# Kernel optimization log

Measured on AMD Instinct MI355X. Metric: run time of the kernel, lower is better.

## Reference

```python
import jax, jax.numpy as jnp
import numpy as np

MATRIC_TYPE = 0   # 0: corr, 1: cov
WEIGHT_IN = 1.0
WEIGHT_BET = 1.0


def setup_inputs() -> dict:
    key = jax.random.key(0)
    k1, k2, k3 = jax.random.split(key, 3)
    x = jax.random.normal(k1, (256, 128, 768), dtype=jnp.float32)
    label = jax.random.randint(k2, (256,), 0, 1000, dtype=jnp.int64 if jax.config.read('jax_enable_x64') else jnp.int32)
    genre_label = jax.random.randint(k3, (256,), 0, 8, dtype=jnp.int64 if jax.config.read('jax_enable_x64') else jnp.int32)
    return {"x": x, "label": label, "genre_label": genre_label}


def _compute_various(x):
    # x: [B, N, D] -> within (D,D), between (D,D)
    B, N, D = x.shape
    tol_num = B * N
    x_mean = jnp.mean(x, axis=1)                       # (B, D)
    mean = jnp.mean(x.reshape(-1, D), axis=0)          # (D,)
    res_x = x - x_mean[:, None, :]                     # (B, N, D)
    # fused batched scatter accumulation (replaces python loop of small mms)
    within = jnp.einsum('bnd,bne->de', res_x, res_x) / tol_num
    res_mean = x_mean - mean                           # (B, D)
    between = (N * (res_mean.T @ res_mean)) / tol_num
    return within, between


def _corr_normalize(m):
    # torch code: Diag=(d,1); mm(Diag.T, Diag)=(1,1) scalar = sum(diag^2)
    d = jnp.diagonal(m)
    s = jnp.sqrt(jnp.sum(d * d))
    return m / s


def reference(x, label, genre_label):
    input_x = x[::2]
    input_u = x[1::2]
    x1_within, x1_between = _compute_various(input_x)
    x2_within, x2_between = _compute_various(input_u)
    if MATRIC_TYPE == 0:
        x1_within = _corr_normalize(x1_within)
        x2_within = _corr_normalize(x2_within)
        x1_between = _corr_normalize(x1_between)
        x2_between = _corr_normalize(x2_between)
    within = jnp.sum((x1_within - x2_within) ** 2)
    between = jnp.sum((x1_between - x2_between) ** 2)
    return WEIGHT_IN * within + WEIGHT_BET * between
```

## Files before the change

### kernel.cpp

```cpp
#include <hip/hip_runtime.h>


typedef float f32x2 __attribute__((ext_vector_type(2)));
typedef float f32x4 __attribute__((ext_vector_type(4)));
typedef short bf16x8 __attribute__((ext_vector_type(8)));
typedef unsigned short u16x4 __attribute__((ext_vector_type(4)));

static constexpr size_t OFF_RT    = 0;
static constexpr size_t OFF_XM    = 50331648;
static constexpr size_t OFF_M     = 51118080;
static constexpr size_t OFF_RM    = 51124224;
static constexpr size_t OFF_P2    = 51517440;
static constexpr size_t OFF_BPART = 54269952;
static constexpr size_t OFF_P1    = 54355968;

__device__ __forceinline__ unsigned int f2bf_u32(float f) {
  union { float f; unsigned int u; } v; v.f = f;
  unsigned int u = v.u;
  unsigned int lsb = (u >> 16) & 1u;
  u += 0x7fffu + lsb;
  return u >> 16;
}

__device__ __forceinline__ void gload_lds16(const void* g, void* l) {
  __builtin_amdgcn_global_load_lds(
      (const __attribute__((address_space(1))) unsigned int*)g,
      (__attribute__((address_space(3))) unsigned int*)l, 16, 0, 0);
}

__global__ void __launch_bounds__(256) k1_means_convert(const float* __restrict__ x,
                                                        float* __restrict__ xm,
                                                        unsigned short* __restrict__ RT) {
  __shared__ unsigned short T[128][130];
  __shared__ float pm[4][128];
  int bid = blockIdx.x;
  int dt = bid % 6, borig = bid / 6;
  int s = borig & 1, b = borig >> 1;
  int tid = threadIdx.x, w = tid >> 6, lane = tid & 63;

  const float* xb = x + (size_t)borig * (128 * 768) + dt * 128 + 2 * lane;
  float cs0 = 0.f, cs1 = 0.f;
#pragma unroll
  for (int g = 0; g < 8; ++g) {
    int n0 = w * 32 + g * 4;
    f32x2 a0 = *reinterpret_cast<const f32x2*>(xb + (size_t)(n0 + 0) * 768);
    f32x2 a1 = *reinterpret_cast<const f32x2*>(xb + (size_t)(n0 + 1) * 768);
    f32x2 a2 = *reinterpret_cast<const f32x2*>(xb + (size_t)(n0 + 2) * 768);
    f32x2 a3 = *reinterpret_cast<const f32x2*>(xb + (size_t)(n0 + 3) * 768);
    cs0 += a0[0] + a1[0] + a2[0] + a3[0];
    cs1 += a0[1] + a1[1] + a2[1] + a3[1];
    u16x4 p0, p1;
    p0[0] = (unsigned short)f2bf_u32(a0[0]); p0[1] = (unsigned short)f2bf_u32(a1[0]);
    p0[2] = (unsigned short)f2bf_u32(a2[0]); p0[3] = (unsigned short)f2bf_u32(a3[0]);
    p1[0] = (unsigned short)f2bf_u32(a0[1]); p1[1] = (unsigned short)f2bf_u32(a1[1]);
    p1[2] = (unsigned short)f2bf_u32(a2[1]); p1[3] = (unsigned short)f2bf_u32(a3[1]);
    *reinterpret_cast<u16x4*>(&T[2 * lane + 0][n0]) = p0;
    *reinterpret_cast<u16x4*>(&T[2 * lane + 1][n0]) = p1;
  }
  *reinterpret_cast<f32x2*>(&pm[w][2 * lane]) = f32x2{cs0, cs1};
  __syncthreads();

  if (tid < 128) {
    float mv = (pm[0][tid] + pm[1][tid] + pm[2][tid] + pm[3][tid]) * (1.f / 128.f);
    xm[((size_t)(s * 128 + b)) * 768ull + dt * 128 + tid] = mv;
  }

  int half = lane >> 5;
  int nb = (lane & 31) * 4;
  unsigned short* rtbase = RT + (size_t)s * (768ull * 16384ull) + (size_t)(b * 128 + nb);
#pragma unroll
  for (int i = 0; i < 16; ++i) {
    int d_loc = w * 32 + 2 * i + half;
    uint2 v = *reinterpret_cast<const uint2*>(&T[d_loc][nb]);
    *reinterpret_cast<uint2*>(rtbase + (size_t)(dt * 128 + d_loc) * 16384ull) = v;
  }
}

__global__ void __launch_bounds__(256) k2_slice_mean(const float* __restrict__ xm,
                                                     float* __restrict__ m,
                                                     unsigned short* __restrict__ rmT) {
  __shared__ float pm[4][64];
  __shared__ float ml[64];
  int s = blockIdx.x / 12, dg = blockIdx.x % 12;
  int t = threadIdx.x;
  int d_loc = t & 63, part = t >> 6;
  int d = dg * 64 + d_loc;
  const float* base = xm + (size_t)s * 128ull * 768ull + d;
  float acc = 0.f;
#pragma unroll 4
  for (int i = 0; i < 32; ++i) acc += base[(size_t)(part * 32 + i) * 768ull];
  pm[part][d_loc] = acc;
  __syncthreads();
  if (t < 64) {
    float mv = (pm[0][t] + pm[1][t] + pm[2][t] + pm[3][t]) * (1.f / 128.f);
    m[s * 768 + dg * 64 + t] = mv;
    ml[t] = mv;
  }
  __syncthreads();
  float mv = ml[d_loc];
  unsigned short* rt = rmT + ((size_t)s * 768ull + d) * 128ull + part * 32;
#pragma unroll 4
  for (int i = 0; i < 32; ++i)
    rt[i] = (unsigned short)f2bf_u32(base[(size_t)(part * 32 + i) * 768ull] - mv);
}

__device__ __forceinline__ void stage_tile(const unsigned short* __restrict__ g, int KP, int k0,
                                           unsigned short* lds, int wave, int lane) {
#pragma unroll
  for (int i = 0; i < 4; ++i) {
    int cb = (i * 4 + wave) * 64;
    int chunk = cb + lane;
    int r = chunk >> 3, sl = chunk & 7;
    int ss = sl ^ (r & 7);
    const unsigned short* src = g + (size_t)r * KP + (k0 + ss * 8);
    gload_lds16(src, lds + (size_t)cb * 8);
  }
}

__device__ __forceinline__ bf16x8 read_frag(const unsigned short* lds, int row, int slot) {
  int chunk = row * 8 + (slot ^ (row & 7));
  return *reinterpret_cast<const bf16x8*>(lds + chunk * 8);
}

__device__ __forceinline__ void tp2tile(int tp, int& td, int& te) {
  td = 0; int t2 = tp;
  while (t2 >= 6 - td) { t2 -= 6 - td; ++td; }
  te = td + t2;
}

__global__ void __launch_bounds__(256) gemm_ata(const unsigned short* __restrict__ Rbig,
                                                const unsigned short* __restrict__ rmT,
                                                float* __restrict__ P1, float* __restrict__ P2,
                                                int ksplit) {
  __shared__ unsigned short Ta[2][128 * 64];
  __shared__ unsigned short Tb[2][128 * 64];
  int bid = blockIdx.x;
  const unsigned short* R; size_t slice_stride; int KP;
  int rest, step0, step1; float* pout;
  if (bid < 42 * ksplit) {
    R = Rbig; slice_stride = 768ull * 16384ull; KP = 16384;
    int c = bid % ksplit; rest = bid / ksplit;
    step0 = (256 * c) / ksplit; step1 = (256 * (c + 1)) / ksplit;
    pout = P1 + (size_t)bid * (128 * 128);
  } else {
    int b2 = bid - 42 * ksplit;
    R = rmT; slice_stride = 768ull * 128ull; KP = 128;
    rest = b2; step0 = 0; step1 = 2;
    pout = P2 + (size_t)b2 * (128 * 128);
  }
  int s = rest & 1; int tp = rest >> 1;
  int td, te; tp2tile(tp, td, te);
  bool diag = (td == te);
  const unsigned short* Ra = R + (size_t)s * slice_stride + (size_t)(td * 128) * KP;
  const unsigned short* Rb = R + (size_t)s * slice_stride + (size_t)(te * 128) * KP;
  int tid = threadIdx.x, wave = tid >> 6, lane = tid & 63;
  int m_off = (wave >> 1) * 64, n_off = (wave & 1) * 64;
  int row_a = m_off + (lane & 15), row_b = n_off + (lane & 15);
  f32x4 acc[4][4];
#pragma unroll
  for (int i = 0; i < 4; ++i)
#pragma unroll
    for (int j = 0; j < 4; ++j) { acc[i][j][0]=0.f; acc[i][j][1]=0.f; acc[i][j][2]=0.f; acc[i][j][3]=0.f; }

  stage_tile(Ra, KP, step0 * 64, Ta[0], wave, lane);
  if (!diag) stage_tile(Rb, KP, step0 * 64, Tb[0], wave, lane);
  __syncthreads();

  int cur = 0;
  for (int kt = step0; kt < step1; ++kt) {
    if (kt + 1 < step1) {
      stage_tile(Ra, KP, (kt + 1) * 64, Ta[cur ^ 1], wave, lane);
      if (!diag) stage_tile(Rb, KP, (kt + 1) * 64, Tb[cur ^ 1], wave, lane);
    }
    const unsigned short* Bsrc = diag ? Ta[cur] : Tb[cur];
#pragma unroll
    for (int ks = 0; ks < 2; ++ks) {
      bf16x8 a[4], b[4];
      int slot = ks * 4 + (lane >> 4);
#pragma unroll
      for (int mi = 0; mi < 4; ++mi) a[mi] = read_frag(Ta[cur], row_a + mi * 16, slot);
#pragma unroll
      for (int ni = 0; ni < 4; ++ni) b[ni] = read_frag(Bsrc, row_b + ni * 16, slot);
#pragma unroll
      for (int mi = 0; mi < 4; ++mi)
#pragma unroll
        for (int ni = 0; ni < 4; ++ni)
          acc[mi][ni] = __builtin_amdgcn_mfma_f32_16x16x32_bf16(a[mi], b[ni], acc[mi][ni], 0, 0, 0);
    }
    __syncthreads();
    cur ^= 1;
  }
  int hi = lane >> 4, lo = lane & 15;
#pragma unroll
  for (int mi = 0; mi < 4; ++mi)
#pragma unroll
    for (int ni = 0; ni < 4; ++ni)
#pragma unroll
      for (int r = 0; r < 4; ++r) {
        int rr = m_off + mi * 16 + hi * 4 + r;
        int cc = n_off + ni * 16 + lo;
        pout[rr * 128 + cc] = acc[mi][ni][r];
      }
}

template <int KS>
__global__ void __launch_bounds__(256) k5_elem(const float* __restrict__ P1,
                                               const float* __restrict__ P2,
                                               const float* __restrict__ m,
                                               float* __restrict__ bpart, int ksplit_rt) {
  __shared__ float red[4][10];
  int bid = blockIdx.x;
  int tp = bid >> 5, sub = bid & 31;
  int td, te; tp2tile(tp, td, te);
  bool diagTile = (td == te);
  float mult = diagTile ? 1.0f : 2.0f;
  int t = threadIdx.x;
  int lane = t & 63, w = t >> 6;
  int ksplit = (KS > 0) ? KS : ksplit_rt;
  float v[10];
#pragma unroll
  for (int j = 0; j < 10; ++j) v[j] = 0.f;

#pragma unroll
  for (int k = 0; k < 2; ++k) {
    int idx = sub * 512 + k * 256 + t;
    int r = idx >> 7, cc = idx & 127;
    int d = td * 128 + r, e = te * 128 + cc;
    float W[2], B[2];
#pragma unroll
    for (int s = 0; s < 2; ++s) {
      const float* base1 = P1 + (size_t)((tp * 2 + s) * ksplit) * 16384ull + idx;
      float g1 = 0.f;
#pragma unroll
      for (int c6 = 0; c6 < ((KS > 0) ? KS : 16); ++c6) {
        if (KS > 0 || c6 < ksplit) g1 += base1[(size_t)c6 * 16384ull];
      }
      float p2v = P2[(size_t)(tp * 2 + s) * 16384ull + idx];
      W[s] = g1 - 128.0f * p2v - 16384.0f * m[s * 768 + d] * m[s * 768 + e];
      B[s] = p2v;
    }
    v[0] += W[0] * W[0] * mult;  v[1] += W[1] * W[1] * mult;  v[2] += W[0] * W[1] * mult;
    v[3] += B[0] * B[0] * mult;  v[4] += B[1] * B[1] * mult;  v[5] += B[0] * B[1] * mult;
    if (diagTile && r == cc) {
      v[6] += W[0] * W[0];  v[7] += W[1] * W[1];
      v[8] += B[0] * B[0];  v[9] += B[1] * B[1];
    }
  }
#pragma unroll
  for (int off = 32; off; off >>= 1)
#pragma unroll
    for (int j = 0; j < 10; ++j) v[j] += __shfl_down(v[j], off, 64);
  if (lane == 0)
#pragma unroll
    for (int j = 0; j < 10; ++j) red[w][j] = v[j];
  __syncthreads();
  if (t < 10) bpart[bid * 16 + t] = red[0][t] + red[1][t] + red[2][t] + red[3][t];
}

__global__ void __launch_bounds__(256) k6_final(const float* __restrict__ bpart,
                                                float* __restrict__ out) {
  __shared__ float red[4][10];
  float acc[10];
#pragma unroll
  for (int j = 0; j < 10; ++j) acc[j] = 0.f;
  for (int i = threadIdx.x; i < 672; i += 256)
#pragma unroll
    for (int j = 0; j < 10; ++j) acc[j] += bpart[i * 16 + j];
  int lane = threadIdx.x & 63, w = threadIdx.x >> 6;
#pragma unroll
  for (int off = 32; off; off >>= 1)
#pragma unroll
    for (int j = 0; j < 10; ++j) acc[j] += __shfl_down(acc[j], off, 64);
  if (lane == 0)
#pragma unroll
    for (int j = 0; j < 10; ++j) red[w][j] = acc[j];
  __syncthreads();
  if (threadIdx.x == 0) {
    float S[10];
#pragma unroll
    for (int j = 0; j < 10; ++j) S[j] = red[0][j] + red[1][j] + red[2][j] + red[3][j];
    float lw = S[0] / S[6] + S[1] / S[7] - 2.0f * S[2] / sqrtf(S[6] * S[7]);
    float lb = S[3] / S[8] + S[4] / S[9] - 2.0f * S[5] / sqrtf(S[8] * S[9]);
    out[0] = lw + lb;
  }
}

extern "C" void kernel_launch(void* const* d_in, const int* in_sizes, int n_in,
                              void* d_out, int out_size, void* d_ws, size_t ws_size,
                              hipStream_t stream) {
  const float* x = (const float*)d_in[0];
  char* ws = (char*)d_ws;
  unsigned short* RT  = (unsigned short*)(ws + OFF_RT);
  float* xm           = (float*)(ws + OFF_XM);
  float* m            = (float*)(ws + OFF_M);
  unsigned short* rmT = (unsigned short*)(ws + OFF_RM);
  float* P2           = (float*)(ws + OFF_P2);
  float* bpart        = (float*)(ws + OFF_BPART);
  float* P1           = (float*)(ws + OFF_P1);
  float* out          = (float*)d_out;

  size_t availP1 = (ws_size > OFF_P1) ? (ws_size - OFF_P1) : 0;
  int ksplit = (int)(availP1 / (42ull * 128 * 128 * 4));
  if (ksplit > 11) ksplit = 11;
  if (ksplit < 1) ksplit = 1;

  hipLaunchKernelGGL(k1_means_convert, dim3(1536), dim3(256), 0, stream, x, xm, RT);
  hipLaunchKernelGGL(k2_slice_mean, dim3(24), dim3(256), 0, stream, xm, m, rmT);
  hipLaunchKernelGGL(gemm_ata, dim3(42 * ksplit + 42), dim3(256), 0, stream,
                     RT, rmT, P1, P2, ksplit);
  if (ksplit == 11) {
    hipLaunchKernelGGL((k5_elem<11>), dim3(672), dim3(256), 0, stream,
                       P1, P2, m, bpart, ksplit);
  } else {
    hipLaunchKernelGGL((k5_elem<0>), dim3(672), dim3(256), 0, stream,
                       P1, P2, m, bpart, ksplit);
  }
  hipLaunchKernelGGL(k6_final, dim3(1), dim3(256), 0, stream, bpart, out);
}
```

Measured before the change: 77.48 us.

## Retile mean/convert kernel so each block writes wider contiguous transposed rows

Each block of the first kernel now covers 32 feature columns across 4 batches (same slice parity) instead of 128 columns of one batch. The transposed bf16 tile is therefore 32 rows by 512 tokens, so the global stores become 16-byte contiguous runs of 1 KB per row rather than 8-byte writes of 256 bytes. The per-column means are reduced with wavefront shuffles instead of a shared-memory partial sum. The cost is narrower 8-byte global reads per lane (16 lanes per row) and a different LDS padding whose bank conflicts may change.

```diff
diff --git a/kernel.cpp b/kernel.cpp
--- a/kernel.cpp
+++ b/kernel.cpp
@@ -31,18 +31,20 @@
 __global__ void __launch_bounds__(256) k1_means_convert(const float* __restrict__ x,
                                                         float* __restrict__ xm,
                                                         unsigned short* __restrict__ RT) {
-  __shared__ unsigned short T[128][130];
-  __shared__ float pm[4][128];
+  __shared__ unsigned short T[32][536];
   int bid = blockIdx.x;
-  int dt = bid % 6, borig = bid / 6;
-  int s = borig & 1, b = borig >> 1;
-  int tid = threadIdx.x, w = tid >> 6, lane = tid & 63;
-
-  const float* xb = x + (size_t)borig * (128 * 768) + dt * 128 + 2 * lane;
+  int dt = bid % 24, rest = bid / 24;
+  int s = rest & 1, bg = rest >> 1;
+  int tid = threadIdx.x, j = tid >> 6, lane = tid & 63;
+  int p = lane & 15, q = lane >> 4;
+  int d0 = dt * 32;
+  int borig = 8 * bg + 2 * j + s;
+
+  const float* xb = x + (size_t)borig * (128 * 768) + d0 + 2 * p;
   float cs0 = 0.f, cs1 = 0.f;
 #pragma unroll
-  for (int g = 0; g < 8; ++g) {
-    int n0 = w * 32 + g * 4;
+  for (int i = 0; i < 8; ++i) {
+    int n0 = i * 16 + q * 4;
     f32x2 a0 = *reinterpret_cast<const f32x2*>(xb + (size_t)(n0 + 0) * 768);
     f32x2 a1 = *reinterpret_cast<const f32x2*>(xb + (size_t)(n0 + 1) * 768);
     f32x2 a2 = *reinterpret_cast<const f32x2*>(xb + (size_t)(n0 + 2) * 768);
@@ -54,25 +56,27 @@
     p0[2] = (unsigned short)f2bf_u32(a2[0]); p0[3] = (unsigned short)f2bf_u32(a3[0]);
     p1[0] = (unsigned short)f2bf_u32(a0[1]); p1[1] = (unsigned short)f2bf_u32(a1[1]);
     p1[2] = (unsigned short)f2bf_u32(a2[1]); p1[3] = (unsigned short)f2bf_u32(a3[1]);
-    *reinterpret_cast<u16x4*>(&T[2 * lane + 0][n0]) = p0;
-    *reinterpret_cast<u16x4*>(&T[2 * lane + 1][n0]) = p1;
-  }
-  *reinterpret_cast<f32x2*>(&pm[w][2 * lane]) = f32x2{cs0, cs1};
-  __syncthreads();
-
-  if (tid < 128) {
-    float mv = (pm[0][tid] + pm[1][tid] + pm[2][tid] + pm[3][tid]) * (1.f / 128.f);
-    xm[((size_t)(s * 128 + b)) * 768ull + dt * 128 + tid] = mv;
-  }
-
-  int half = lane >> 5;
-  int nb = (lane & 31) * 4;
-  unsigned short* rtbase = RT + (size_t)s * (768ull * 16384ull) + (size_t)(b * 128 + nb);
-#pragma unroll
-  for (int i = 0; i < 16; ++i) {
-    int d_loc = w * 32 + 2 * i + half;
-    uint2 v = *reinterpret_cast<const uint2*>(&T[d_loc][nb]);
-    *reinterpret_cast<uint2*>(rtbase + (size_t)(dt * 128 + d_loc) * 16384ull) = v;
+    int col = j * 128 + n0;
+    *reinterpret_cast<u16x4*>(&T[2 * p + 0][col]) = p0;
+    *reinterpret_cast<u16x4*>(&T[2 * p + 1][col]) = p1;
+  }
+  cs0 += __shfl_xor(cs0, 16, 64);  cs0 += __shfl_xor(cs0, 32, 64);
+  cs1 += __shfl_xor(cs1, 16, 64);  cs1 += __shfl_xor(cs1, 32, 64);
+  if (q == 0) {
+    int b = bg * 4 + j;
+    f32x2 mv; mv[0] = cs0 * (1.f / 128.f); mv[1] = cs1 * (1.f / 128.f);
+    *reinterpret_cast<f32x2*>(xm + (size_t)(s * 128 + b) * 768ull + d0 + 2 * p) = mv;
+  }
+  __syncthreads();
+
+  int r = tid >> 3, cb = tid & 7;
+  unsigned short* rtrow = RT + (size_t)s * (768ull * 16384ull)
+                             + (size_t)(d0 + r) * 16384ull + (size_t)bg * 512;
+#pragma unroll
+  for (int k = 0; k < 8; ++k) {
+    int c = cb + k * 8;
+    uint4 v = *reinterpret_cast<const uint4*>(&T[r][c * 8]);
+    *reinterpret_cast<uint4*>(rtrow + c * 8) = v;
   }
 }
 
```

After: 78.47 us. No clear change (+1.3%).
